# Kernel tuning notes

Measured on AMD Instinct MI355X. Metric: run time of the kernel, lower is better.

Reference implementation:

```python
import jax, jax.numpy as jnp
import numpy as np

HIDDEN = 1024
NUM_EXPERTS = 8
TOP_K = 2
B, S = 4, 2048


def setup_inputs() -> dict:
    key = jax.random.key(0)
    ks = jax.random.split(key, 7)
    s = 0.02
    return {
        "x": jax.random.normal(ks[0], (B, S, HIDDEN), dtype=jnp.float32),
        "gate_w": jax.random.normal(ks[1], (NUM_EXPERTS, HIDDEN), dtype=jnp.float32) * s,
        "gate_b": jnp.zeros((NUM_EXPERTS,), dtype=jnp.float32),
        "w1": jax.random.normal(ks[2], (NUM_EXPERTS, 4 * HIDDEN, HIDDEN), dtype=jnp.float32) * s,
        "b1": jnp.zeros((NUM_EXPERTS, 4 * HIDDEN), dtype=jnp.float32),
        "w2": jax.random.normal(ks[3], (NUM_EXPERTS, HIDDEN, 4 * HIDDEN), dtype=jnp.float32) * s,
        "b2": jnp.zeros((NUM_EXPERTS, HIDDEN), dtype=jnp.float32),
    }


def reference(x, gate_w, gate_b, w1, b1, w2, b2):
    bsz, seq_len, hidden = x.shape
    T = bsz * seq_len
    flat = x.reshape(T, hidden)  # [T, H]

    gate_logits = flat @ gate_w.T + gate_b  # [T, E]
    topk_vals, topk_idx = jax.lax.top_k(gate_logits, TOP_K)  # [T, K]
    topk_w = jax.nn.softmax(topk_vals, axis=-1)  # [T, K]

    # combine[t, e] = routing weight of expert e for token t (0 if not selected)
    combine = jnp.zeros((T, NUM_EXPERTS), dtype=flat.dtype)
    combine = combine.at[jnp.arange(T)[:, None], topk_idx].add(topk_w)

    out_flat = jnp.zeros_like(flat)
    for e in range(NUM_EXPERTS):  # small fixed expert count
        h = jax.nn.gelu(flat @ w1[e].T + b1[e], approximate=False)  # [T, 4H]
        y = h @ w2[e].T + b2[e]  # [T, H]
        out_flat = out_flat + y * combine[:, e:e + 1]

    out = out_flat.reshape(bsz, seq_len, hidden)
    probs = jax.nn.softmax(gate_logits, axis=-1).mean(axis=0)  # [E]
    l_aux = (probs * probs).sum() * NUM_EXPERTS
    return out, l_aux
```

## Files before the change

kernel.cpp:

```cpp
#include <hip/hip_runtime.h>
#include <cstdint>
#include <cstddef>

typedef unsigned short u16;
typedef short bf16x8 __attribute__((ext_vector_type(8)));
typedef float f32x4 __attribute__((ext_vector_type(4)));
typedef u16 u16x4 __attribute__((ext_vector_type(4)));

#define NTOK 8192
#define HID 1024
#define NEXP 8
#define FF 4096
#define FCHUNK 1024
#define NCHUNK 4
#define MAXPAIR 17408
#define BM 128
#define BN 128
#define BK 64

__device__ __forceinline__ u16 bf16_rne(float f) {
  unsigned u = __builtin_bit_cast(unsigned, f);
  return (u16)((u + 0x7FFFu + ((u >> 16) & 1u)) >> 16);
}

__device__ __forceinline__ float gelu_tanh(float v) {
  const float u = 0.7978845608028654f * (v + 0.044715f * v * v * v);
  const float e = __expf(2.0f * u);
  return v - v * __frcp_rn(e + 1.0f);
}

__device__ __forceinline__ void async16(const void* g, void* l) {
  __builtin_amdgcn_global_load_lds(
      (const __attribute__((address_space(1))) void*)g,
      (__attribute__((address_space(3))) void*)l, 16, 0, 0);
}

__global__ __launch_bounds__(256) void gate_kernel(
    const float* __restrict__ x, const float* __restrict__ gw,
    const float* __restrict__ gb, int* __restrict__ counts,
    float* __restrict__ probs_sum, int* __restrict__ topk_e,
    float* __restrict__ topk_w) {
  __shared__ float sgw[NEXP * HID];
  __shared__ float sProbs[NEXP];
  __shared__ int sCnt[NEXP];
  const int tid = threadIdx.x;
  for (int i = tid; i < NEXP * HID; i += 256) sgw[i] = gw[i];
  if (tid < NEXP) { sProbs[tid] = 0.f; sCnt[tid] = 0; }
  __syncthreads();
  const int lane = tid & 63, wave = tid >> 6;
  for (int it = 0; it < 4; ++it) {
    const int t = blockIdx.x * 16 + wave * 4 + it;
    const float* xr = x + (size_t)t * HID;
    float a[NEXP];
#pragma unroll
    for (int e = 0; e < NEXP; ++e) a[e] = 0.f;
    for (int j = 0; j < 16; ++j) {
      const int o = lane + 64 * j;
      const float v = xr[o];
#pragma unroll
      for (int e = 0; e < NEXP; ++e) a[e] += v * sgw[e * HID + o];
    }
#pragma unroll
    for (int off = 32; off > 0; off >>= 1)
#pragma unroll
      for (int e = 0; e < NEXP; ++e) a[e] += __shfl_xor(a[e], off);
    if (lane == 0) {
      float l[NEXP];
#pragma unroll
      for (int e = 0; e < NEXP; ++e) l[e] = a[e] + gb[e];
      int b0 = 0; float v0 = l[0];
#pragma unroll
      for (int e = 1; e < NEXP; ++e) if (l[e] > v0) { b0 = e; v0 = l[e]; }
      int b1i = (b0 == 0) ? 1 : 0; float v1 = l[b1i];
#pragma unroll
      for (int e = 0; e < NEXP; ++e) if (e != b0 && l[e] > v1) { b1i = e; v1 = l[e]; }
      const float e1 = __expf(v1 - v0);
      const float inv01 = 1.f / (1.f + e1);
      topk_e[2 * t] = b0; topk_e[2 * t + 1] = b1i;
      topk_w[2 * t] = inv01; topk_w[2 * t + 1] = e1 * inv01;
      atomicAdd(&sCnt[b0], 1); atomicAdd(&sCnt[b1i], 1);
      float s = 0.f, p[NEXP];
#pragma unroll
      for (int e = 0; e < NEXP; ++e) { p[e] = __expf(l[e] - v0); s += p[e]; }
      const float invs = 1.f / s;
#pragma unroll
      for (int e = 0; e < NEXP; ++e) atomicAdd(&sProbs[e], p[e] * invs);
    }
  }
  __syncthreads();
  if (tid < NEXP) {
    atomicAdd(&counts[tid], sCnt[tid]);
    atomicAdd(&probs_sum[tid], sProbs[tid]);
  }
}

__global__ void finalize_kernel(const int* __restrict__ counts,
                                int* __restrict__ cursors,
                                int* __restrict__ offsets,
                                const float* __restrict__ probs_sum,
                                float* __restrict__ laux) {
  if (threadIdx.x == 0) {
    int off = 0;
    for (int e = 0; e < NEXP; ++e) {
      offsets[e] = off;
      off += ((counts[e] + (BM - 1)) / BM) * BM;
      cursors[e] = 0;
    }
    offsets[NEXP] = off;
    float s = 0.f;
    for (int e = 0; e < NEXP; ++e) {
      const float p = probs_sum[e] * (1.f / (float)NTOK);
      s += p * p;
    }
    *laux = (float)NEXP * s;
  }
}

__global__ __launch_bounds__(256) void scatter_kernel(
    const int* __restrict__ topk_e, const float* __restrict__ topk_w,
    const int* __restrict__ offsets, int* __restrict__ cursors,
    int* __restrict__ tok_of_pair, float* __restrict__ wt_of_pair,
    int* __restrict__ slot_of_tok) {
  __shared__ int lcnt[NEXP], lbase[NEXP];
  const int tid = threadIdx.x;
  if (tid < NEXP) lcnt[tid] = 0;
  __syncthreads();
  const int t = blockIdx.x * 256 + tid;
  const int e0 = topk_e[2 * t], e1 = topk_e[2 * t + 1];
  const int p0 = atomicAdd(&lcnt[e0], 1);
  const int p1 = atomicAdd(&lcnt[e1], 1);
  __syncthreads();
  if (tid < NEXP) lbase[tid] = atomicAdd(&cursors[tid], lcnt[tid]);
  __syncthreads();
  const int s0 = offsets[e0] + lbase[e0] + p0;
  const int s1 = offsets[e1] + lbase[e1] + p1;
  tok_of_pair[s0] = t; wt_of_pair[s0] = topk_w[2 * t];
  tok_of_pair[s1] = t; wt_of_pair[s1] = topk_w[2 * t + 1];
  slot_of_tok[2 * t] = s0; slot_of_tok[2 * t + 1] = s1;
}

__global__ __launch_bounds__(256) void stream_cvt_kernel(const float4* __restrict__ src,
                                                         u16x4* __restrict__ dst) {
  const int i = blockIdx.x * 256 + threadIdx.x;
  const float4 v = src[i];
  u16x4 o;
  o[0] = bf16_rne(v.x); o[1] = bf16_rne(v.y); o[2] = bf16_rne(v.z); o[3] = bf16_rne(v.w);
  dst[i] = o;
}

__global__ __launch_bounds__(256) void cvt_w1_kernel(const float4* __restrict__ w1,
                                                     u16x4* __restrict__ w1b, int c) {
  const int i = blockIdx.x * 256 + threadIdx.x;
  const int e = i >> 18;
  const int r = i & 262143;
  const float4 v = w1[(size_t)e * 1048576 + (size_t)c * 262144 + r];
  u16x4 o;
  o[0] = bf16_rne(v.x); o[1] = bf16_rne(v.y); o[2] = bf16_rne(v.z); o[3] = bf16_rne(v.w);
  w1b[i] = o;
}

__global__ __launch_bounds__(256) void cvt_w2_kernel(const float4* __restrict__ w2,
                                                     u16x4* __restrict__ w2b, int c) {
  const int i = blockIdx.x * 256 + threadIdx.x;
  const int e = i >> 18;
  const int r = i & 262143;
  const int o = r >> 8;
  const int j4 = r & 255;
  const float4 v = w2[(size_t)e * 1048576 + (size_t)o * 1024 + (size_t)c * 256 + j4];
  u16x4 ov;
  ov[0] = bf16_rne(v.x); ov[1] = bf16_rne(v.y); ov[2] = bf16_rne(v.z); ov[3] = bf16_rne(v.w);
  w2b[i] = ov;
}


__global__ __launch_bounds__(256) void pass1_kernel(
    const u16* __restrict__ xb, const u16* __restrict__ w1b,
    const float* __restrict__ b1, const int* __restrict__ tok_of_pair,
    const int* __restrict__ offsets, u16* __restrict__ h, const int ffN,
    const int chunk) {
  __shared__ u16 As[BM * BK];
  __shared__ u16 Bs[BN * BK];
  const int nt = blockIdx.x, mt = blockIdx.y;
  const int base = mt * BM;
  if (base >= offsets[NEXP]) return;
  int e = 0;
  while (e < NEXP - 1 && base >= offsets[e + 1]) ++e;
  const int tid = threadIdx.x;
  const int lane = tid & 63;
  const int wave = tid >> 6;
  const int wm = wave & 1, wn = wave >> 1;
  const int srow = tid >> 3;
  const int scol = (tid & 7) * 8;
  const int scolg = (((tid & 7) ^ ((tid >> 3) & 7)) * 8);
  int tokA[4];
#pragma unroll
  for (int i = 0; i < 4; ++i) tokA[i] = tok_of_pair[base + i * 32 + srow];
  const u16* wB = w1b + (size_t)e * ((size_t)ffN * HID) + (size_t)(nt * BN) * HID;
  f32x4 acc[4][4];
#pragma unroll
  for (int i = 0; i < 4; ++i)
#pragma unroll
    for (int j = 0; j < 4; ++j) acc[i][j] = (f32x4){0.f, 0.f, 0.f, 0.f};

  for (int k0 = 0; k0 < HID; k0 += BK) {
#pragma unroll
    for (int i = 0; i < 4; ++i) {
      async16(xb + (size_t)tokA[i] * HID + k0 + scolg, &As[(i * 32 + srow) * BK + scol]);
      async16(wB + (size_t)(i * 32 + srow) * HID + k0 + scolg, &Bs[(i * 32 + srow) * BK + scol]);
    }
    __syncthreads();
    const int nl = lane & 15;
    const int q = lane >> 4;
    const int sw = nl & 7;
#pragma unroll
    for (int s = 0; s < 2; ++s) {
      const int kg = ((s * 4 + q) ^ sw) * 8;
      bf16x8 af[4], bf[4];
#pragma unroll
      for (int i = 0; i < 4; ++i)
        af[i] = *(const bf16x8*)&As[(wm * 64 + i * 16 + nl) * BK + kg];
#pragma unroll
      for (int j = 0; j < 4; ++j)
        bf[j] = *(const bf16x8*)&Bs[(wn * 64 + j * 16 + nl) * BK + kg];
#pragma unroll
      for (int i = 0; i < 4; ++i)
#pragma unroll
        for (int j = 0; j < 4; ++j)
          acc[i][j] = __builtin_amdgcn_mfma_f32_16x16x32_bf16(af[i], bf[j], acc[i][j], 0, 0, 0);
    }
    __syncthreads();
  }
  const int nl = lane & 15;
  const int rowq = (lane >> 4) * 4;
  const float* b1e = b1 + (size_t)e * FF + (size_t)chunk * FCHUNK;
#pragma unroll
  for (int i = 0; i < 4; ++i) {
#pragma unroll
    for (int j = 0; j < 4; ++j) {
      const int n = nt * BN + wn * 64 + j * 16 + nl;
      const float bias = b1e[n];
#pragma unroll
      for (int r = 0; r < 4; ++r) {
        const int m = base + wm * 64 + i * 16 + rowq + r;
        h[(size_t)m * ffN + n] = bf16_rne(gelu_tanh(acc[i][j][r] + bias));
      }
    }
  }
}

template <bool YP>
__global__ __launch_bounds__(256) void pass2_kernel(
    const u16* __restrict__ h, const u16* __restrict__ w2b,
    const float* __restrict__ b2, const int* __restrict__ tok_of_pair,
    const float* __restrict__ wt_of_pair, const int* __restrict__ offsets,
    float* __restrict__ ypair, float* __restrict__ out, const int kTot,
    const int chunk) {
  __shared__ u16 As[BM * BK];
  __shared__ u16 Bs[BN * BK];
  const int nt = blockIdx.x, mt = blockIdx.y;
  const int base = mt * BM;
  if (base >= offsets[NEXP]) return;
  int e = 0;
  while (e < NEXP - 1 && base >= offsets[e + 1]) ++e;
  const int tid = threadIdx.x;
  const int lane = tid & 63;
  const int wave = tid >> 6;
  const int wm = wave & 1, wn = wave >> 1;
  const int srow = tid >> 3;
  const int scol = (tid & 7) * 8;
  const int scolg = (((tid & 7) ^ ((tid >> 3) & 7)) * 8);
  const u16* wB = w2b + (size_t)e * ((size_t)HID * kTot) + (size_t)(nt * BN) * kTot;
  f32x4 acc[4][4];
#pragma unroll
  for (int i = 0; i < 4; ++i)
#pragma unroll
    for (int j = 0; j < 4; ++j) acc[i][j] = (f32x4){0.f, 0.f, 0.f, 0.f};

  for (int k0 = 0; k0 < kTot; k0 += BK) {
#pragma unroll
    for (int i = 0; i < 4; ++i) {
      async16(h + (size_t)(base + i * 32 + srow) * kTot + k0 + scolg,
              &As[(i * 32 + srow) * BK + scol]);
      async16(wB + (size_t)(i * 32 + srow) * kTot + k0 + scolg,
              &Bs[(i * 32 + srow) * BK + scol]);
    }
    __syncthreads();
    const int nl = lane & 15;
    const int q = lane >> 4;
    const int sw = nl & 7;
#pragma unroll
    for (int s = 0; s < 2; ++s) {
      const int kg = ((s * 4 + q) ^ sw) * 8;
      bf16x8 af[4], bf[4];
#pragma unroll
      for (int i = 0; i < 4; ++i)
        af[i] = *(const bf16x8*)&As[(wm * 64 + i * 16 + nl) * BK + kg];
#pragma unroll
      for (int j = 0; j < 4; ++j)
        bf[j] = *(const bf16x8*)&Bs[(wn * 64 + j * 16 + nl) * BK + kg];
#pragma unroll
      for (int i = 0; i < 4; ++i)
#pragma unroll
        for (int j = 0; j < 4; ++j)
          acc[i][j] = __builtin_amdgcn_mfma_f32_16x16x32_bf16(af[i], bf[j], acc[i][j], 0, 0, 0);
    }
    __syncthreads();
  }
  const int nl = lane & 15;
  const int rowq = (lane >> 4) * 4;
  if (YP) {
#pragma unroll
    for (int i = 0; i < 4; ++i) {
#pragma unroll
      for (int r = 0; r < 4; ++r) {
        const int m = base + wm * 64 + i * 16 + rowq + r;
        float* yrow = ypair + (size_t)m * HID;
#pragma unroll
        for (int j = 0; j < 4; ++j) {
          const int o = nt * BN + wn * 64 + j * 16 + nl;
          float v = acc[i][j][r];
          if (chunk != 0) v += yrow[o];
          yrow[o] = v;
        }
      }
    }
  } else {
    const float* b2e = b2 + (size_t)e * HID;
#pragma unroll
    for (int i = 0; i < 4; ++i) {
#pragma unroll
      for (int r = 0; r < 4; ++r) {
        const int m = base + wm * 64 + i * 16 + rowq + r;
        const int tokm = tok_of_pair[m];
        const float wtm = wt_of_pair[m];
        float* orow = out + (size_t)tokm * HID;
#pragma unroll
        for (int j = 0; j < 4; ++j) {
          const int o = nt * BN + wn * 64 + j * 16 + nl;
          float v = acc[i][j][r];
          if (chunk == 0) v += b2e[o];
          atomicAdd(&orow[o], wtm * v);
        }
      }
    }
  }
}

__global__ __launch_bounds__(256) void combine_kernel(
    const float* __restrict__ ypair, const int* __restrict__ slot_of_tok,
    const int* __restrict__ topk_e, const float* __restrict__ topk_w,
    const float* __restrict__ b2, float* __restrict__ out) {
  const int t = blockIdx.x;
  const int tid = threadIdx.x;
  const int s0 = slot_of_tok[2 * t], s1 = slot_of_tok[2 * t + 1];
  const int e0 = topk_e[2 * t], e1 = topk_e[2 * t + 1];
  const float w0 = topk_w[2 * t], w1v = topk_w[2 * t + 1];
  const float4 y0 = ((const float4*)(ypair + (size_t)s0 * HID))[tid];
  const float4 y1 = ((const float4*)(ypair + (size_t)s1 * HID))[tid];
  const float4 c0 = ((const float4*)(b2 + (size_t)e0 * HID))[tid];
  const float4 c1 = ((const float4*)(b2 + (size_t)e1 * HID))[tid];
  float4 o;
  o.x = w0 * (y0.x + c0.x) + w1v * (y1.x + c1.x);
  o.y = w0 * (y0.y + c0.y) + w1v * (y1.y + c1.y);
  o.z = w0 * (y0.z + c0.z) + w1v * (y1.z + c1.z);
  o.w = w0 * (y0.w + c0.w) + w1v * (y1.w + c1.w);
  ((float4*)(out + (size_t)t * HID))[tid] = o;
}

extern "C" void kernel_launch(void* const* d_in, const int* in_sizes, int n_in,
                              void* d_out, int out_size, void* d_ws, size_t ws_size,
                              hipStream_t stream) {
  (void)in_sizes; (void)n_in;
  const float* x  = (const float*)d_in[0];
  const float* gw = (const float*)d_in[1];
  const float* gb = (const float*)d_in[2];
  const float* w1 = (const float*)d_in[3];
  const float* b1 = (const float*)d_in[4];
  const float* w2 = (const float*)d_in[5];
  const float* b2 = (const float*)d_in[6];
  float* out = (float*)d_out;

  char* ws = (char*)d_ws;
  int*   counts  = (int*)(ws + 0);
  int*   cursors = (int*)(ws + 32);
  float* probs   = (float*)(ws + 64);
  int*   offsets = (int*)(ws + 96);
  int*   tok     = (int*)(ws + 256);
  float* wt      = (float*)(ws + 256 + 4 * MAXPAIR);
  int*   topk_e  = (int*)(ws + 139520);
  float* topk_w  = (float*)(ws + 205056);
  int*   slot    = (int*)(ws + 270592);
  const size_t OFF_XB = 336128;
  u16* xb = (u16*)(ws + OFF_XB);

  const size_t OFF_W1B_F = OFF_XB + 16777216;
  const size_t OFF_W2B_F = OFF_W1B_F + 67108864;
  const size_t OFF_H_F   = OFF_W2B_F + 67108864;
  const size_t OFF_YP_F  = OFF_H_F + (size_t)MAXPAIR * FF * 2;
  const size_t WS_FULL_AT = OFF_YP_F;
  const size_t WS_FULL_YP = OFF_YP_F + (size_t)MAXPAIR * HID * 4;

  const size_t OFF_W1B_C = OFF_XB + 16777216;
  const size_t OFF_W2B_C = OFF_W1B_C + 16777216;
  const size_t OFF_H_C   = OFF_W2B_C + 16777216;
  const size_t OFF_YP_C  = OFF_H_C + (size_t)MAXPAIR * FCHUNK * 2;
  const size_t WS_CHUNK_YP = OFF_YP_C + (size_t)MAXPAIR * HID * 4;

  hipMemsetAsync(ws, 0, 139520, stream);

  gate_kernel<<<512, 256, 0, stream>>>(x, gw, gb, counts, probs, topk_e, topk_w);
  finalize_kernel<<<1, 64, 0, stream>>>(counts, cursors, offsets, probs,
                                        out + (out_size - 1));
  scatter_kernel<<<32, 256, 0, stream>>>(topk_e, topk_w, offsets, cursors, tok, wt, slot);
  stream_cvt_kernel<<<8192, 256, 0, stream>>>((const float4*)x, (u16x4*)xb);

  if (ws_size >= WS_FULL_AT) {
    const bool yp = ws_size >= WS_FULL_YP;
    u16*   w1b   = (u16*)(ws + OFF_W1B_F);
    u16*   w2b   = (u16*)(ws + OFF_W2B_F);
    u16*   hbuf  = (u16*)(ws + OFF_H_F);
    float* ypair = (float*)(ws + OFF_YP_F);
    if (!yp) hipMemsetAsync(d_out, 0, (size_t)out_size * 4, stream);

    stream_cvt_kernel<<<32768, 256, 0, stream>>>((const float4*)w1, (u16x4*)w1b);
    stream_cvt_kernel<<<32768, 256, 0, stream>>>((const float4*)w2, (u16x4*)w2b);
    pass1_kernel<<<dim3(FF / BN, 136), 256, 0, stream>>>(xb, w1b, b1, tok, offsets,
                                                         hbuf, FF, 0);
    if (yp) {
      pass2_kernel<true><<<dim3(HID / BN, 136), 256, 0, stream>>>(
          hbuf, w2b, b2, tok, wt, offsets, ypair, out, FF, 0);
      combine_kernel<<<8192, 256, 0, stream>>>(ypair, slot, topk_e, topk_w, b2, out);
    } else {
      pass2_kernel<false><<<dim3(HID / BN, 136), 256, 0, stream>>>(
          hbuf, w2b, b2, tok, wt, offsets, ypair, out, FF, 0);
    }
  } else {
    const bool yp = ws_size >= WS_CHUNK_YP;
    u16*   w1b   = (u16*)(ws + OFF_W1B_C);
    u16*   w2b   = (u16*)(ws + OFF_W2B_C);
    u16*   hbuf  = (u16*)(ws + OFF_H_C);
    float* ypair = (float*)(ws + OFF_YP_C);
    if (!yp) hipMemsetAsync(d_out, 0, (size_t)out_size * 4, stream);

    for (int c = 0; c < NCHUNK; ++c) {
      cvt_w1_kernel<<<8192, 256, 0, stream>>>((const float4*)w1, (u16x4*)w1b, c);
      pass1_kernel<<<dim3(FCHUNK / BN, 136), 256, 0, stream>>>(xb, w1b, b1, tok, offsets,
                                                               hbuf, FCHUNK, c);
      cvt_w2_kernel<<<8192, 256, 0, stream>>>((const float4*)w2, (u16x4*)w2b, c);
      if (yp)
        pass2_kernel<true><<<dim3(HID / BN, 136), 256, 0, stream>>>(
            hbuf, w2b, b2, tok, wt, offsets, ypair, out, FCHUNK, c);
      else
        pass2_kernel<false><<<dim3(HID / BN, 136), 256, 0, stream>>>(
            hbuf, w2b, b2, tok, wt, offsets, ypair, out, FCHUNK, c);
    }
    if (yp)
      combine_kernel<<<8192, 256, 0, stream>>>(ypair, slot, topk_e, topk_w, b2, out);
  }
}
```

Before: 904.3 us.

## Replace pass1/pass2 with a 256x256 multi-stage pipelined MoE GEMM kernel

Replaces the two 128x128 grouped GEMM kernels with one templated 512-thread kernel. It uses 256x256 output tiles, a 4-deep LDS ring with async global-to-LDS prefetch two steps ahead, split barriers and s_setprio around the MFMA bursts. Expert padding grows to 256 rows and the workspace-size fallbacks (chunked and atomic paths) are removed, so the full bf16 weight conversion and ypair combine path always run. The aim is more data reuse per tile and loads overlapped with compute, at the cost of more padding waste, higher register and LDS use, and reliance on a large workspace. ypair aliases the xb region, which is only safe because xb is consumed before pass 2.

Result: faster. 878.1 us (-2.9%).

```diff
diff --git a/kernel.cpp b/kernel.cpp
--- a/kernel.cpp
+++ b/kernel.cpp
@@ -11,12 +11,7 @@
 #define HID 1024
 #define NEXP 8
 #define FF 4096
-#define FCHUNK 1024
-#define NCHUNK 4
-#define MAXPAIR 17408
-#define BM 128
-#define BN 128
-#define BK 64
+#define MAXPAIR 18432
 
 __device__ __forceinline__ u16 bf16_rne(float f) {
   unsigned u = __builtin_bit_cast(unsigned, f);
@@ -103,7 +98,7 @@
     int off = 0;
     for (int e = 0; e < NEXP; ++e) {
       offsets[e] = off;
-      off += ((counts[e] + (BM - 1)) / BM) * BM;
+      off += ((counts[e] + 255) / 256) * 256;
       cursors[e] = 0;
     }
     offsets[NEXP] = off;
@@ -148,40 +143,22 @@
   dst[i] = o;
 }
 
-__global__ __launch_bounds__(256) void cvt_w1_kernel(const float4* __restrict__ w1,
-                                                     u16x4* __restrict__ w1b, int c) {
-  const int i = blockIdx.x * 256 + threadIdx.x;
-  const int e = i >> 18;
-  const int r = i & 262143;
-  const float4 v = w1[(size_t)e * 1048576 + (size_t)c * 262144 + r];
-  u16x4 o;
-  o[0] = bf16_rne(v.x); o[1] = bf16_rne(v.y); o[2] = bf16_rne(v.z); o[3] = bf16_rne(v.w);
-  w1b[i] = o;
-}
-
-__global__ __launch_bounds__(256) void cvt_w2_kernel(const float4* __restrict__ w2,
-                                                     u16x4* __restrict__ w2b, int c) {
-  const int i = blockIdx.x * 256 + threadIdx.x;
-  const int e = i >> 18;
-  const int r = i & 262143;
-  const int o = r >> 8;
-  const int j4 = r & 255;
-  const float4 v = w2[(size_t)e * 1048576 + (size_t)o * 1024 + (size_t)c * 256 + j4];
-  u16x4 ov;
-  ov[0] = bf16_rne(v.x); ov[1] = bf16_rne(v.y); ov[2] = bf16_rne(v.z); ov[3] = bf16_rne(v.w);
-  w2b[i] = ov;
-}
-
-
-__global__ __launch_bounds__(256) void pass1_kernel(
-    const u16* __restrict__ xb, const u16* __restrict__ w1b,
-    const float* __restrict__ b1, const int* __restrict__ tok_of_pair,
-    const int* __restrict__ offsets, u16* __restrict__ h, const int ffN,
-    const int chunk) {
-  __shared__ u16 As[BM * BK];
-  __shared__ u16 Bs[BN * BK];
+template <bool P1>
+__global__ __launch_bounds__(512, 2) void moe_gemm(
+    const u16* __restrict__ Aop,
+    const u16* __restrict__ Bop,
+    const float* __restrict__ b1,
+    const int* __restrict__ tok_of_pair,
+    const int* __restrict__ offsets,
+    u16* __restrict__ hout,
+    float* __restrict__ ypair) {
+  constexpr int LDK  = P1 ? HID : FF;
+  constexpr int NOUT = P1 ? FF : HID;
+  constexpr int T    = LDK / 32;
+  __shared__ u16 As[4][8192];
+  __shared__ u16 Bs[4][8192];
   const int nt = blockIdx.x, mt = blockIdx.y;
-  const int base = mt * BM;
+  const int base = mt * 256;
   if (base >= offsets[NEXP]) return;
   int e = 0;
   while (e < NEXP - 1 && base >= offsets[e + 1]) ++e;
@@ -189,158 +166,111 @@
   const int lane = tid & 63;
   const int wave = tid >> 6;
   const int wm = wave & 1, wn = wave >> 1;
-  const int srow = tid >> 3;
-  const int scol = (tid & 7) * 8;
-  const int scolg = (((tid & 7) ^ ((tid >> 3) & 7)) * 8);
-  int tokA[4];
-#pragma unroll
-  for (int i = 0; i < 4; ++i) tokA[i] = tok_of_pair[base + i * 32 + srow];
-  const u16* wB = w1b + (size_t)e * ((size_t)ffN * HID) + (size_t)(nt * BN) * HID;
-  f32x4 acc[4][4];
-#pragma unroll
-  for (int i = 0; i < 4; ++i)
+
+  const int gl = (tid & 7) ^ ((tid >> 3) & 7);
+  const int rS = ((tid >> 3) << 1) | (gl >> 2);
+  const int cS = (gl & 3) * 8;
+  const u16 *gA0, *gA1;
+  if constexpr (P1) {
+    gA0 = Aop + (size_t)tok_of_pair[base + rS] * LDK + cS;
+    gA1 = Aop + (size_t)tok_of_pair[base + rS + 128] * LDK + cS;
+  } else {
+    gA0 = Aop + (size_t)(base + rS) * LDK + cS;
+    gA1 = Aop + (size_t)(base + rS + 128) * LDK + cS;
+  }
+  const u16* wBb = Bop + (size_t)e * ((size_t)NOUT * LDK) + (size_t)(nt * 256) * LDK;
+  const u16* gB0 = wBb + (size_t)rS * LDK + cS;
+  const u16* gB1 = wBb + (size_t)(rS + 128) * LDK + cS;
+
+#define STAGE_A(step) { u16* d_ = &As[(step) & 3][0]; const int k_ = (step) * 32; \
+    async16(gA0 + k_, d_ + (size_t)tid * 8); async16(gA1 + k_, d_ + ((size_t)tid + 512) * 8); }
+#define STAGE_B(step) { u16* d_ = &Bs[(step) & 3][0]; const int k_ = (step) * 32; \
+    async16(gB0 + k_, d_ + (size_t)tid * 8); async16(gB1 + k_, d_ + ((size_t)tid + 512) * 8); }
+
+  STAGE_A(0); STAGE_B(0); STAGE_A(1); STAGE_B(1);
+  asm volatile("s_waitcnt vmcnt(4)" ::: "memory");
+  __builtin_amdgcn_s_barrier();
+  __builtin_amdgcn_sched_barrier(0);
+
+  const int nl = lane & 15, q = lane >> 4;
+  const int rdS = (((((nl & 1) << 2) | q) ^ (nl >> 1))) * 8;
+  const int aB = (wm * 64 + (nl >> 1)) * 64 + rdS;
+  const int bB = (wn * 32 + (nl >> 1)) * 64 + rdS;
+
+  f32x4 acc[8][4];
+#pragma unroll
+  for (int i = 0; i < 8; ++i)
 #pragma unroll
     for (int j = 0; j < 4; ++j) acc[i][j] = (f32x4){0.f, 0.f, 0.f, 0.f};
 
-  for (int k0 = 0; k0 < HID; k0 += BK) {
-#pragma unroll
-    for (int i = 0; i < 4; ++i) {
-      async16(xb + (size_t)tokA[i] * HID + k0 + scolg, &As[(i * 32 + srow) * BK + scol]);
-      async16(wB + (size_t)(i * 32 + srow) * HID + k0 + scolg, &Bs[(i * 32 + srow) * BK + scol]);
-    }
-    __syncthreads();
-    const int nl = lane & 15;
-    const int q = lane >> 4;
-    const int sw = nl & 7;
-#pragma unroll
-    for (int s = 0; s < 2; ++s) {
-      const int kg = ((s * 4 + q) ^ sw) * 8;
-      bf16x8 af[4], bf[4];
-#pragma unroll
-      for (int i = 0; i < 4; ++i)
-        af[i] = *(const bf16x8*)&As[(wm * 64 + i * 16 + nl) * BK + kg];
+#pragma unroll 1
+  for (int t = 0; t < T; ++t) {
+    const u16* A = &As[t & 3][0];
+    const u16* B = &Bs[t & 3][0];
+    const bool pf = (t + 2 < T);
+    bf16x8 af[4], bf[4];
+#pragma unroll
+    for (int i = 0; i < 4; ++i) af[i] = *(const bf16x8*)&A[aB + i * 512];
+#pragma unroll
+    for (int j = 0; j < 4; ++j) bf[j] = *(const bf16x8*)&B[bB + j * 512];
+    if (pf) STAGE_A(t + 2);
+    __builtin_amdgcn_s_barrier();
+    __builtin_amdgcn_sched_barrier(0);
+    __builtin_amdgcn_s_setprio(1);
+#pragma unroll
+    for (int i = 0; i < 4; ++i)
 #pragma unroll
       for (int j = 0; j < 4; ++j)
-        bf[j] = *(const bf16x8*)&Bs[(wn * 64 + j * 16 + nl) * BK + kg];
-#pragma unroll
-      for (int i = 0; i < 4; ++i)
-#pragma unroll
-        for (int j = 0; j < 4; ++j)
-          acc[i][j] = __builtin_amdgcn_mfma_f32_16x16x32_bf16(af[i], bf[j], acc[i][j], 0, 0, 0);
-    }
-    __syncthreads();
-  }
-  const int nl = lane & 15;
-  const int rowq = (lane >> 4) * 4;
-  const float* b1e = b1 + (size_t)e * FF + (size_t)chunk * FCHUNK;
-#pragma unroll
-  for (int i = 0; i < 4; ++i) {
+        acc[i][j] = __builtin_amdgcn_mfma_f32_16x16x32_bf16(af[i], bf[j], acc[i][j], 0, 0, 0);
+    __builtin_amdgcn_s_setprio(0);
+    __builtin_amdgcn_s_barrier();
+    __builtin_amdgcn_sched_barrier(0);
+#pragma unroll
+    for (int i = 0; i < 4; ++i) af[i] = *(const bf16x8*)&A[aB + 2048 + i * 512];
+    if (pf) STAGE_B(t + 2);
+    __builtin_amdgcn_s_barrier();
+    __builtin_amdgcn_sched_barrier(0);
+    __builtin_amdgcn_s_setprio(1);
+#pragma unroll
+    for (int i = 0; i < 4; ++i)
+#pragma unroll
+      for (int j = 0; j < 4; ++j)
+        acc[4 + i][j] = __builtin_amdgcn_mfma_f32_16x16x32_bf16(af[i], bf[j], acc[4 + i][j], 0, 0, 0);
+    __builtin_amdgcn_s_setprio(0);
+    if (t + 1 < T) {
+      if (pf) { asm volatile("s_waitcnt vmcnt(4)" ::: "memory"); }
+      else    { asm volatile("s_waitcnt vmcnt(0)" ::: "memory"); }
+    }
+    __builtin_amdgcn_s_barrier();
+    __builtin_amdgcn_sched_barrier(0);
+  }
+#undef STAGE_A
+#undef STAGE_B
+
+  const int rowq = q * 4;
+  if constexpr (P1) {
+    const float* b1e = b1 + (size_t)e * FF;
 #pragma unroll
     for (int j = 0; j < 4; ++j) {
-      const int n = nt * BN + wn * 64 + j * 16 + nl;
+      const int n = nt * 256 + wn * 64 + j * 16 + nl;
       const float bias = b1e[n];
 #pragma unroll
+      for (int i = 0; i < 8; ++i) {
+        const int m = base + wm * 128 + i * 16 + rowq;
+#pragma unroll
+        for (int r = 0; r < 4; ++r)
+          hout[(size_t)(m + r) * FF + n] = bf16_rne(gelu_tanh(acc[i][j][r] + bias));
+      }
+    }
+  } else {
+#pragma unroll
+    for (int i = 0; i < 8; ++i) {
+      const int m = base + wm * 128 + i * 16 + rowq;
+#pragma unroll
       for (int r = 0; r < 4; ++r) {
-        const int m = base + wm * 64 + i * 16 + rowq + r;
-        h[(size_t)m * ffN + n] = bf16_rne(gelu_tanh(acc[i][j][r] + bias));
-      }
-    }
-  }
-}
-
-template <bool YP>
-__global__ __launch_bounds__(256) void pass2_kernel(
-    const u16* __restrict__ h, const u16* __restrict__ w2b,
-    const float* __restrict__ b2, const int* __restrict__ tok_of_pair,
-    const float* __restrict__ wt_of_pair, const int* __restrict__ offsets,
-    float* __restrict__ ypair, float* __restrict__ out, const int kTot,
-    const int chunk) {
-  __shared__ u16 As[BM * BK];
-  __shared__ u16 Bs[BN * BK];
-  const int nt = blockIdx.x, mt = blockIdx.y;
-  const int base = mt * BM;
-  if (base >= offsets[NEXP]) return;
-  int e = 0;
-  while (e < NEXP - 1 && base >= offsets[e + 1]) ++e;
-  const int tid = threadIdx.x;
-  const int lane = tid & 63;
-  const int wave = tid >> 6;
-  const int wm = wave & 1, wn = wave >> 1;
-  const int srow = tid >> 3;
-  const int scol = (tid & 7) * 8;
-  const int scolg = (((tid & 7) ^ ((tid >> 3) & 7)) * 8);
-  const u16* wB = w2b + (size_t)e * ((size_t)HID * kTot) + (size_t)(nt * BN) * kTot;
-  f32x4 acc[4][4];
-#pragma unroll
-  for (int i = 0; i < 4; ++i)
-#pragma unroll
-    for (int j = 0; j < 4; ++j) acc[i][j] = (f32x4){0.f, 0.f, 0.f, 0.f};
-
-  for (int k0 = 0; k0 < kTot; k0 += BK) {
-#pragma unroll
-    for (int i = 0; i < 4; ++i) {
-      async16(h + (size_t)(base + i * 32 + srow) * kTot + k0 + scolg,
-              &As[(i * 32 + srow) * BK + scol]);
-      async16(wB + (size_t)(i * 32 + srow) * kTot + k0 + scolg,
-              &Bs[(i * 32 + srow) * BK + scol]);
-    }
-    __syncthreads();
-    const int nl = lane & 15;
-    const int q = lane >> 4;
-    const int sw = nl & 7;
-#pragma unroll
-    for (int s = 0; s < 2; ++s) {
-      const int kg = ((s * 4 + q) ^ sw) * 8;
-      bf16x8 af[4], bf[4];
-#pragma unroll
-      for (int i = 0; i < 4; ++i)
-        af[i] = *(const bf16x8*)&As[(wm * 64 + i * 16 + nl) * BK + kg];
-#pragma unroll
-      for (int j = 0; j < 4; ++j)
-        bf[j] = *(const bf16x8*)&Bs[(wn * 64 + j * 16 + nl) * BK + kg];
-#pragma unroll
-      for (int i = 0; i < 4; ++i)
-#pragma unroll
-        for (int j = 0; j < 4; ++j)
-          acc[i][j] = __builtin_amdgcn_mfma_f32_16x16x32_bf16(af[i], bf[j], acc[i][j], 0, 0, 0);
-    }
-    __syncthreads();
-  }
-  const int nl = lane & 15;
-  const int rowq = (lane >> 4) * 4;
-  if (YP) {
-#pragma unroll
-    for (int i = 0; i < 4; ++i) {
-#pragma unroll
-      for (int r = 0; r < 4; ++r) {
-        const int m = base + wm * 64 + i * 16 + rowq + r;
-        float* yrow = ypair + (size_t)m * HID;
-#pragma unroll
-        for (int j = 0; j < 4; ++j) {
-          const int o = nt * BN + wn * 64 + j * 16 + nl;
-          float v = acc[i][j][r];
-          if (chunk != 0) v += yrow[o];
-          yrow[o] = v;
-        }
-      }
-    }
-  } else {
-    const float* b2e = b2 + (size_t)e * HID;
-#pragma unroll
-    for (int i = 0; i < 4; ++i) {
-#pragma unroll
-      for (int r = 0; r < 4; ++r) {
-        const int m = base + wm * 64 + i * 16 + rowq + r;
-        const int tokm = tok_of_pair[m];
-        const float wtm = wt_of_pair[m];
-        float* orow = out + (size_t)tokm * HID;
-#pragma unroll
-        for (int j = 0; j < 4; ++j) {
-          const int o = nt * BN + wn * 64 + j * 16 + nl;
-          float v = acc[i][j][r];
-          if (chunk == 0) v += b2e[o];
-          atomicAdd(&orow[o], wtm * v);
-        }
+        float* yrow = ypair + (size_t)(m + r) * HID + nt * 256 + wn * 64;
+#pragma unroll
+        for (int j = 0; j < 4; ++j) yrow[j * 16 + nl] = acc[i][j][r];
       }
     }
   }
@@ -370,7 +300,7 @@
 extern "C" void kernel_launch(void* const* d_in, const int* in_sizes, int n_in,
                               void* d_out, int out_size, void* d_ws, size_t ws_size,
                               hipStream_t stream) {
-  (void)in_sizes; (void)n_in;
+  (void)in_sizes; (void)n_in; (void)ws_size;
   const float* x  = (const float*)d_in[0];
   const float* gw = (const float*)d_in[1];
   const float* gb = (const float*)d_in[2];
@@ -385,76 +315,31 @@
   int*   cursors = (int*)(ws + 32);
   float* probs   = (float*)(ws + 64);
   int*   offsets = (int*)(ws + 96);
-  int*   tok     = (int*)(ws + 256);
-  float* wt      = (float*)(ws + 256 + 4 * MAXPAIR);
-  int*   topk_e  = (int*)(ws + 139520);
-  float* topk_w  = (float*)(ws + 205056);
-  int*   slot    = (int*)(ws + 270592);
-  const size_t OFF_XB = 336128;
-  u16* xb = (u16*)(ws + OFF_XB);
-
-  const size_t OFF_W1B_F = OFF_XB + 16777216;
-  const size_t OFF_W2B_F = OFF_W1B_F + 67108864;
-  const size_t OFF_H_F   = OFF_W2B_F + 67108864;
-  const size_t OFF_YP_F  = OFF_H_F + (size_t)MAXPAIR * FF * 2;
-  const size_t WS_FULL_AT = OFF_YP_F;
-  const size_t WS_FULL_YP = OFF_YP_F + (size_t)MAXPAIR * HID * 4;
-
-  const size_t OFF_W1B_C = OFF_XB + 16777216;
-  const size_t OFF_W2B_C = OFF_W1B_C + 16777216;
-  const size_t OFF_H_C   = OFF_W2B_C + 16777216;
-  const size_t OFF_YP_C  = OFF_H_C + (size_t)MAXPAIR * FCHUNK * 2;
-  const size_t WS_CHUNK_YP = OFF_YP_C + (size_t)MAXPAIR * HID * 4;
-
-  hipMemsetAsync(ws, 0, 139520, stream);
+  int*   tok     = (int*)(ws + 4096);
+  float* wt      = (float*)(ws + 77824);
+  int*   topk_e  = (int*)(ws + 151552);
+  float* topk_w  = (float*)(ws + 217088);
+  int*   slot    = (int*)(ws + 282624);
+  u16*   xb    = (u16*)(ws + 1048576);
+  u16*   w1b   = (u16*)(ws + 17825792);
+  u16*   w2b   = (u16*)(ws + 84934656);
+  u16*   hbuf  = (u16*)(ws + 152043520);
+  float* ypair = (float*)(ws + 1048576);
+
+  hipMemsetAsync(ws, 0, 348160, stream);
 
   gate_kernel<<<512, 256, 0, stream>>>(x, gw, gb, counts, probs, topk_e, topk_w);
   finalize_kernel<<<1, 64, 0, stream>>>(counts, cursors, offsets, probs,
                                         out + (out_size - 1));
   scatter_kernel<<<32, 256, 0, stream>>>(topk_e, topk_w, offsets, cursors, tok, wt, slot);
   stream_cvt_kernel<<<8192, 256, 0, stream>>>((const float4*)x, (u16x4*)xb);
-
-  if (ws_size >= WS_FULL_AT) {
-    const bool yp = ws_size >= WS_FULL_YP;
-    u16*   w1b   = (u16*)(ws + OFF_W1B_F);
-    u16*   w2b   = (u16*)(ws + OFF_W2B_F);
-    u16*   hbuf  = (u16*)(ws + OFF_H_F);
-    float* ypair = (float*)(ws + OFF_YP_F);
-    if (!yp) hipMemsetAsync(d_out, 0, (size_t)out_size * 4, stream);
-
-    stream_cvt_kernel<<<32768, 256, 0, stream>>>((const float4*)w1, (u16x4*)w1b);
-    stream_cvt_kernel<<<32768, 256, 0, stream>>>((const float4*)w2, (u16x4*)w2b);
-    pass1_kernel<<<dim3(FF / BN, 136), 256, 0, stream>>>(xb, w1b, b1, tok, offsets,
-                                                         hbuf, FF, 0);
-    if (yp) {
-      pass2_kernel<true><<<dim3(HID / BN, 136), 256, 0, stream>>>(
-          hbuf, w2b, b2, tok, wt, offsets, ypair, out, FF, 0);
-      combine_kernel<<<8192, 256, 0, stream>>>(ypair, slot, topk_e, topk_w, b2, out);
-    } else {
-      pass2_kernel<false><<<dim3(HID / BN, 136), 256, 0, stream>>>(
-          hbuf, w2b, b2, tok, wt, offsets, ypair, out, FF, 0);
-    }
-  } else {
-    const bool yp = ws_size >= WS_CHUNK_YP;
-    u16*   w1b   = (u16*)(ws + OFF_W1B_C);
-    u16*   w2b   = (u16*)(ws + OFF_W2B_C);
-    u16*   hbuf  = (u16*)(ws + OFF_H_C);
-    float* ypair = (float*)(ws + OFF_YP_C);
-    if (!yp) hipMemsetAsync(d_out, 0, (size_t)out_size * 4, stream);
-
-    for (int c = 0; c < NCHUNK; ++c) {
-      cvt_w1_kernel<<<8192, 256, 0, stream>>>((const float4*)w1, (u16x4*)w1b, c);
-      pass1_kernel<<<dim3(FCHUNK / BN, 136), 256, 0, stream>>>(xb, w1b, b1, tok, offsets,
-                                                               hbuf, FCHUNK, c);
-      cvt_w2_kernel<<<8192, 256, 0, stream>>>((const float4*)w2, (u16x4*)w2b, c);
-      if (yp)
-        pass2_kernel<true><<<dim3(HID / BN, 136), 256, 0, stream>>>(
-            hbuf, w2b, b2, tok, wt, offsets, ypair, out, FCHUNK, c);
-      else
-        pass2_kernel<false><<<dim3(HID / BN, 136), 256, 0, stream>>>(
-            hbuf, w2b, b2, tok, wt, offsets, ypair, out, FCHUNK, c);
-    }
-    if (yp)
-      combine_kernel<<<8192, 256, 0, stream>>>(ypair, slot, topk_e, topk_w, b2, out);
-  }
-}
+  stream_cvt_kernel<<<32768, 256, 0, stream>>>((const float4*)w1, (u16x4*)w1b);
+  stream_cvt_kernel<<<32768, 256, 0, stream>>>((const float4*)w2, (u16x4*)w2b);
+
+  const int MT = MAXPAIR / 256;
+  moe_gemm<true><<<dim3(FF / 256, MT), 512, 0, stream>>>(
+      xb, w1b, b1, tok, offsets, hbuf, nullptr);
+  moe_gemm<false><<<dim3(HID / 256, MT), 512, 0, stream>>>(
+      hbuf, w2b, nullptr, tok, offsets, nullptr, ypair);
+  combine_kernel<<<8192, 256, 0, stream>>>(ypair, slot, topk_e, topk_w, b2, out);
+}
```
